# Performance work log

Hardware: AMD Instinct MI355X
Metric: run time of the kernel (lower is better)

Reference implementation:

```python
import jax, jax.numpy as jnp
import numpy as np

B, T, N, C = 1, 2, 10000, 64
H, Co = 4, 64
E = 160000
NEG_SLOPE = 0.2
LN_EPS = 1e-5


def setup_inputs() -> dict:
    key = jax.random.key(0)
    ks = jax.random.split(key, 8)
    s_in = 1.0 / np.sqrt(C)
    s_att = 1.0 / np.sqrt(Co)
    s_proj = 1.0 / np.sqrt(H * Co)
    return {
        "x": jax.random.normal(ks[0], (B, T, N, C), jnp.float32),
        "edge_index": jax.random.randint(ks[1], (2, E), 0, N, dtype=jnp.int32),
        "W_l": jax.random.normal(ks[2], (C, H * Co), jnp.float32) * s_in,
        "b_l": jnp.zeros((H * Co,), jnp.float32),
        "W_r": jax.random.normal(ks[3], (C, H * Co), jnp.float32) * s_in,
        "b_r": jnp.zeros((H * Co,), jnp.float32),
        "att": jax.random.normal(ks[4], (H, Co), jnp.float32) * s_att,
        "bias": jnp.zeros((H * Co,), jnp.float32),
        "W_proj": jax.random.normal(ks[5], (H * Co, Co), jnp.float32) * s_proj,
        "b_proj": jnp.zeros((Co,), jnp.float32),
        "ln_gamma": jnp.ones((Co,), jnp.float32),
        "ln_beta": jnp.zeros((Co,), jnp.float32),
    }


def reference(x, edge_index, W_l, b_l, W_r, b_r, att, bias, W_proj, b_proj, ln_gamma, ln_beta):
    src, dst = edge_index[0], edge_index[1]
    # node transforms: [B,T,N,H,Co]
    x_l = (x @ W_l + b_l).reshape(B, T, N, H, Co)
    x_r = (x @ W_r + b_r).reshape(B, T, N, H, Co)
    # per-edge gathers: [B,T,E,H,Co]
    x_j = x_l[:, :, src]  # source-side features (messages)
    x_i = x_r[:, :, dst]  # target-side features
    m = jax.nn.leaky_relu(x_i + x_j, NEG_SLOPE)
    alpha = jnp.einsum('bteho,ho->bteh', m, att)  # [B,T,E,H]
    # segment softmax over edges grouped by target node (edge axis leading)
    a = jnp.moveaxis(alpha, 2, 0)  # [E,B,T,H]
    amax = jax.lax.stop_gradient(jax.ops.segment_max(a, dst, num_segments=N))
    a = jnp.exp(a - amax[dst])
    denom = jax.ops.segment_sum(a, dst, num_segments=N)
    attn = a / denom[dst]  # [E,B,T,H]
    # weighted messages scattered to target nodes
    msg = jnp.moveaxis(x_j, 2, 0) * attn[..., None]  # [E,B,T,H,Co]
    agg = jax.ops.segment_sum(msg, dst, num_segments=N)  # [N,B,T,H,Co]
    out = jnp.moveaxis(agg, 0, 2).reshape(B, T, N, H * Co) + bias
    x_mha = jax.nn.relu(out)
    # projection + identity residual (in_channels == out_channels)
    x_sam = x_mha @ W_proj + b_proj + x
    mu = jnp.mean(x_sam, axis=-1, keepdims=True)
    var = jnp.var(x_sam, axis=-1, keepdims=True)
    y = (x_sam - mu) * jax.lax.rsqrt(var + LN_EPS) * ln_gamma + ln_beta
    return jax.nn.relu(y)
```

## Files before the change

kernel.cpp:

```cpp
#include <hip/hip_runtime.h>

#define T_  2
#define N_  10000
#define C_  64
#define H_  4
#define Co_ 64
#define E_  160000
#define HC_ 256
#define PAD_ 48
#define NEG_SLOPE 0.2f
#define LN_EPS 1e-5f
#define SCAT_BLOCKS (E_ / 256)
#define GEMM_BLOCKS (T_ * N_ / 32)

typedef float v2f __attribute__((ext_vector_type(2)));
typedef unsigned short bfx8 __attribute__((ext_vector_type(8)));

#if __has_builtin(__builtin_elementwise_fma)
#define PKFMA(a, b, c) __builtin_elementwise_fma((a), (b), (c))
#else
#define PKFMA(a, b, c) ((a) * (b) + (c))
#endif

__device__ __forceinline__ v2f v2(float x, float y) { v2f r; r.x = x; r.y = y; return r; }
__device__ __forceinline__ v2f sp(float x) { v2f r; r.x = x; r.y = x; return r; }

__device__ __forceinline__ float bf2f(unsigned short u) {
    return __uint_as_float((unsigned)u << 16);
}
__device__ __forceinline__ unsigned short f2bf(float f) {
    const unsigned u = __float_as_uint(f);
    return (unsigned short)((u + 0x7FFFu + ((u >> 16) & 1u)) >> 16);
}

__device__ __forceinline__ void red8x2(float& p0, float& p1) {
    asm("s_nop 1\n\t"
        "v_add_f32_dpp %0, %0, %0 quad_perm:[1,0,3,2] row_mask:0xf bank_mask:0xf\n\t"
        "v_add_f32_dpp %1, %1, %1 quad_perm:[1,0,3,2] row_mask:0xf bank_mask:0xf\n\t"
        "s_nop 0\n\t"
        "v_add_f32_dpp %0, %0, %0 quad_perm:[2,3,0,1] row_mask:0xf bank_mask:0xf\n\t"
        "v_add_f32_dpp %1, %1, %1 quad_perm:[2,3,0,1] row_mask:0xf bank_mask:0xf\n\t"
        "s_nop 0\n\t"
        "v_add_f32_dpp %0, %0, %0 row_half_mirror row_mask:0xf bank_mask:0xf\n\t"
        "v_add_f32_dpp %1, %1, %1 row_half_mirror row_mask:0xf bank_mask:0xf"
        : "+v"(p0), "+v"(p1));
}

__global__ __launch_bounds__(256) void scat_gemm(
        const int* __restrict__ src, const int* __restrict__ dst,
        int* __restrict__ cursor, unsigned short* __restrict__ perm,
        const float* __restrict__ x, const float* __restrict__ Wl,
        const float* __restrict__ bl, const float* __restrict__ Wr,
        const float* __restrict__ br, unsigned short* __restrict__ xlb,
        float* __restrict__ xr) {
    __shared__ float4 xs[32 * 16];
    const int tid = threadIdx.x;
    if (blockIdx.x < SCAT_BLOCKS) {
        const int e = blockIdx.x * 256 + tid;
        const int d = dst[e];
        const int pos = atomicAdd(&cursor[d], 1);
        if (pos < PAD_) perm[d * PAD_ + pos] = (unsigned short)src[e];
        return;
    }
    const int r0 = (blockIdx.x - SCAT_BLOCKS) * 32;
    xs[tid]       = ((const float4*)(x + (size_t)r0 * C_))[tid];
    xs[256 + tid] = ((const float4*)(x + (size_t)r0 * C_))[256 + tid];
    __syncthreads();

    const int wv    = tid >> 6;
    const int mat   = wv >> 1;
    const int rbase = (wv & 1) << 4;
    const int col4  = tid & 63;
    const float* W  = mat ? Wr : Wl;
    const float4 b4 = ((const float4*)(mat ? br : bl))[col4];

    v2f accA[16], accB[16];
    #pragma unroll
    for (int r = 0; r < 16; ++r) { accA[r] = v2(b4.x, b4.y); accB[r] = v2(b4.z, b4.w); }

    #pragma unroll 2
    for (int c4 = 0; c4 < 16; ++c4) {
        const float4 w0 = ((const float4*)(W + (size_t)(c4 * 4 + 0) * HC_))[col4];
        const float4 w1 = ((const float4*)(W + (size_t)(c4 * 4 + 1) * HC_))[col4];
        const float4 w2 = ((const float4*)(W + (size_t)(c4 * 4 + 2) * HC_))[col4];
        const float4 w3 = ((const float4*)(W + (size_t)(c4 * 4 + 3) * HC_))[col4];
        const v2f w0A = v2(w0.x, w0.y), w0B = v2(w0.z, w0.w);
        const v2f w1A = v2(w1.x, w1.y), w1B = v2(w1.z, w1.w);
        const v2f w2A = v2(w2.x, w2.y), w2B = v2(w2.z, w2.w);
        const v2f w3A = v2(w3.x, w3.y), w3B = v2(w3.z, w3.w);
        #pragma unroll
        for (int r = 0; r < 16; ++r) {
            const float4 xv = xs[(rbase + r) * 16 + c4];
            accA[r] = PKFMA(sp(xv.x), w0A, accA[r]);
            accB[r] = PKFMA(sp(xv.x), w0B, accB[r]);
            accA[r] = PKFMA(sp(xv.y), w1A, accA[r]);
            accB[r] = PKFMA(sp(xv.y), w1B, accB[r]);
            accA[r] = PKFMA(sp(xv.z), w2A, accA[r]);
            accB[r] = PKFMA(sp(xv.z), w2B, accB[r]);
            accA[r] = PKFMA(sp(xv.w), w3A, accA[r]);
            accB[r] = PKFMA(sp(xv.w), w3B, accB[r]);
        }
    }
    if (mat) {
        #pragma unroll
        for (int r = 0; r < 16; ++r) {
            float4 o4;
            o4.x = accA[r].x; o4.y = accA[r].y; o4.z = accB[r].x; o4.w = accB[r].y;
            ((float4*)(xr + (size_t)(r0 + rbase + r) * HC_))[col4] = o4;
        }
    } else {
        #pragma unroll
        for (int r = 0; r < 16; ++r) {
            ushort4 u;
            u.x = f2bf(accA[r].x); u.y = f2bf(accA[r].y);
            u.z = f2bf(accB[r].x); u.w = f2bf(accB[r].y);
            ((ushort4*)(xlb + (size_t)(r0 + rbase + r) * HC_))[col4] = u;
        }
    }
}

__global__ __launch_bounds__(128, 6) void node_proj(
        const unsigned short* __restrict__ xlb, const float* __restrict__ xr,
        const float* __restrict__ att, const unsigned short* __restrict__ perm,
        const int* __restrict__ cursor, const float* __restrict__ bias,
        const float* __restrict__ Wp, const float* __restrict__ bp,
        const float* __restrict__ x, const float* __restrict__ gamma,
        const float* __restrict__ beta, float* __restrict__ out) {
    __shared__ float sh_act[T_][HC_];
    __shared__ float sh_part[T_][T_][Co_];
    const int t    = threadIdx.x >> 6;
    const int lane = threadIdx.x & 63;
    const int q    = lane & 31;
    const int half = lane >> 5;
    const int n    = blockIdx.x;
    const int deg  = min(cursor[n], PAD_);
    const int lim  = deg - half;
    const size_t row = (size_t)t * N_ + n;

    const float4 xiA = ((const float4*)&xr[row * HC_])[2 * q];
    const float4 xiB = ((const float4*)&xr[row * HC_])[2 * q + 1];
    const float4 avA = ((const float4*)att)[2 * q];
    const float4 avB = ((const float4*)att)[2 * q + 1];
    const v2f X0 = v2(xiA.x, xiA.y), X1 = v2(xiA.z, xiA.w);
    const v2f X2 = v2(xiB.x, xiB.y), X3 = v2(xiB.z, xiB.w);
    const float L2E = 1.44269504f;
    const v2f A0v = v2(avA.x * L2E, avA.y * L2E), A1v = v2(avA.z * L2E, avA.w * L2E);
    const v2f A2v = v2(avB.x * L2E, avB.y * L2E), A3v = v2(avB.z * L2E, avB.w * L2E);

    const int myidx = (lane < deg) ? (int)perm[n * PAD_ + lane] : 0;
    const unsigned short* xlt = xlb + (size_t)t * N_ * HC_;

    float s = 0.f;
    v2f ac0 = v2(0.f, 0.f), ac1 = ac0, ac2 = ac0, ac3 = ac0;

    bfx8 Au, Bu, Cu, Du;
    auto fetchA = [&](int kk) {
        const int i0 = __builtin_amdgcn_readlane(myidx, kk + 0);
        const int i1 = __builtin_amdgcn_readlane(myidx, kk + 1);
        const int i2 = __builtin_amdgcn_readlane(myidx, kk + 2);
        const int i3 = __builtin_amdgcn_readlane(myidx, kk + 3);
        const int ia = half ? i1 : i0;
        const int ib = half ? i3 : i2;
        Au = *(const bfx8*)&xlt[(size_t)ia * HC_ + 8 * q];
        Bu = *(const bfx8*)&xlt[(size_t)ib * HC_ + 8 * q];
    };
    auto fetchB = [&](int kk) {
        const int i0 = __builtin_amdgcn_readlane(myidx, kk + 0);
        const int i1 = __builtin_amdgcn_readlane(myidx, kk + 1);
        const int i2 = __builtin_amdgcn_readlane(myidx, kk + 2);
        const int i3 = __builtin_amdgcn_readlane(myidx, kk + 3);
        const int ia = half ? i1 : i0;
        const int ib = half ? i3 : i2;
        Cu = *(const bfx8*)&xlt[(size_t)ia * HC_ + 8 * q];
        Du = *(const bfx8*)&xlt[(size_t)ib * HC_ + 8 * q];
    };
    auto pair_update = [&](const bfx8 u0, const bfx8 u1, int kbase) {
        const v2f c00 = v2(bf2f(u0[0]), bf2f(u0[1]));
        const v2f c01 = v2(bf2f(u0[2]), bf2f(u0[3]));
        const v2f c02 = v2(bf2f(u0[4]), bf2f(u0[5]));
        const v2f c03 = v2(bf2f(u0[6]), bf2f(u0[7]));
        const v2f c10 = v2(bf2f(u1[0]), bf2f(u1[1]));
        const v2f c11 = v2(bf2f(u1[2]), bf2f(u1[3]));
        const v2f c12 = v2(bf2f(u1[4]), bf2f(u1[5]));
        const v2f c13 = v2(bf2f(u1[6]), bf2f(u1[7]));
        v2f u, l, P;
        u = c00 + X0; l = __builtin_elementwise_max(u, u * NEG_SLOPE); P = l * A0v;
        u = c01 + X1; l = __builtin_elementwise_max(u, u * NEG_SLOPE); P = PKFMA(l, A1v, P);
        u = c02 + X2; l = __builtin_elementwise_max(u, u * NEG_SLOPE); P = PKFMA(l, A2v, P);
        u = c03 + X3; l = __builtin_elementwise_max(u, u * NEG_SLOPE); P = PKFMA(l, A3v, P);
        float p0 = P.x + P.y;
        u = c10 + X0; l = __builtin_elementwise_max(u, u * NEG_SLOPE); P = l * A0v;
        u = c11 + X1; l = __builtin_elementwise_max(u, u * NEG_SLOPE); P = PKFMA(l, A1v, P);
        u = c12 + X2; l = __builtin_elementwise_max(u, u * NEG_SLOPE); P = PKFMA(l, A2v, P);
        u = c13 + X3; l = __builtin_elementwise_max(u, u * NEG_SLOPE); P = PKFMA(l, A3v, P);
        float p1 = P.x + P.y;
        p0 = (kbase < lim)     ? p0 : -INFINITY;
        p1 = (kbase + 2 < lim) ? p1 : -INFINITY;
        red8x2(p0, p1);
        const float w0 = exp2f(p0);
        const float w1 = exp2f(p1);
        s += w0 + w1;
        ac0 = PKFMA(c00, sp(w0), ac0); ac0 = PKFMA(c10, sp(w1), ac0);
        ac1 = PKFMA(c01, sp(w0), ac1); ac1 = PKFMA(c11, sp(w1), ac1);
        ac2 = PKFMA(c02, sp(w0), ac2); ac2 = PKFMA(c12, sp(w1), ac2);
        ac3 = PKFMA(c03, sp(w0), ac3); ac3 = PKFMA(c13, sp(w1), ac3);
    };
    if (deg > 0) fetchA(0);
    if (deg > 4) fetchB(4);
    for (int k = 0; k < deg; k += 8) {
        {
            const bfx8 u0 = Au, u1 = Bu;
            if (k + 8 < deg) fetchA(k + 8);
            pair_update(u0, u1, k);
        }
        if (k + 4 < deg) {
            const bfx8 u0 = Cu, u1 = Du;
            if (k + 12 < deg) fetchB(k + 12);
            pair_update(u0, u1, k + 4);
        }
    }

    s += __shfl_xor(s, 32, 64);
    ac0.x += __shfl_xor(ac0.x, 32, 64); ac0.y += __shfl_xor(ac0.y, 32, 64);
    ac1.x += __shfl_xor(ac1.x, 32, 64); ac1.y += __shfl_xor(ac1.y, 32, 64);
    ac2.x += __shfl_xor(ac2.x, 32, 64); ac2.y += __shfl_xor(ac2.y, 32, 64);
    ac3.x += __shfl_xor(ac3.x, 32, 64); ac3.y += __shfl_xor(ac3.y, 32, 64);

    if (lane < 32) {
        const float inv = (deg > 0) ? 1.f / s : 0.f;
        const float4 bA = ((const float4*)bias)[2 * q];
        const float4 bB = ((const float4*)bias)[2 * q + 1];
        float4 vA, vB;
        vA.x = fmaxf(fmaf(ac0.x, inv, bA.x), 0.f);
        vA.y = fmaxf(fmaf(ac0.y, inv, bA.y), 0.f);
        vA.z = fmaxf(fmaf(ac1.x, inv, bA.z), 0.f);
        vA.w = fmaxf(fmaf(ac1.y, inv, bA.w), 0.f);
        vB.x = fmaxf(fmaf(ac2.x, inv, bB.x), 0.f);
        vB.y = fmaxf(fmaf(ac2.y, inv, bB.y), 0.f);
        vB.z = fmaxf(fmaf(ac3.x, inv, bB.z), 0.f);
        vB.w = fmaxf(fmaf(ac3.y, inv, bB.w), 0.f);
        ((float4*)&sh_act[t][0])[2 * q]     = vA;
        ((float4*)&sh_act[t][0])[2 * q + 1] = vB;
    }
    __syncthreads();

    v2f P0 = v2(0.f, 0.f), P1 = v2(0.f, 0.f);
    {
        const int kq = t * 32;
        #pragma unroll 4
        for (int k4 = 0; k4 < 32; ++k4) {
            const int k = (kq + k4) * 4;
            const float w0 = Wp[(size_t)(k + 0) * Co_ + lane];
            const float w1 = Wp[(size_t)(k + 1) * Co_ + lane];
            const float w2 = Wp[(size_t)(k + 2) * Co_ + lane];
            const float w3 = Wp[(size_t)(k + 3) * Co_ + lane];
            const v2f w01 = v2(w0, w1), w23 = v2(w2, w3);
            const float4 a0 = ((const float4*)&sh_act[0][0])[kq + k4];
            const float4 a1 = ((const float4*)&sh_act[1][0])[kq + k4];
            P0 = PKFMA(v2(a0.x, a0.y), w01, P0);
            P0 = PKFMA(v2(a0.z, a0.w), w23, P0);
            P1 = PKFMA(v2(a1.x, a1.y), w01, P1);
            P1 = PKFMA(v2(a1.z, a1.w), w23, P1);
        }
    }
    sh_part[t][0][lane] = P0.x + P0.y;
    sh_part[t][1][lane] = P1.x + P1.y;
    __syncthreads();

    const int o = lane;
    float p = sh_part[0][t][o] + sh_part[1][t][o]
            + bp[o] + x[((size_t)t * N_ + n) * C_ + o];
    const float go = gamma[o], bo = beta[o];
    float s1r = p;
    #pragma unroll
    for (int off = 1; off < 64; off <<= 1) s1r += __shfl_xor(s1r, off, 64);
    const float mu = s1r * (1.f / 64.f);
    const float dv = p - mu;
    float s2r = dv * dv;
    #pragma unroll
    for (int off = 1; off < 64; off <<= 1) s2r += __shfl_xor(s2r, off, 64);
    out[((size_t)t * N_ + n) * C_ + o] =
        fmaxf(dv * rsqrtf(s2r * (1.f / 64.f) + LN_EPS) * go + bo, 0.f);
}

extern "C" void kernel_launch(void* const* d_in, const int* in_sizes, int n_in,
                              void* d_out, int out_size, void* d_ws, size_t ws_size,
                              hipStream_t stream) {
    const float* x    = (const float*)d_in[0];
    const int*   ei   = (const int*)  d_in[1];
    const float* Wl   = (const float*)d_in[2];
    const float* bl   = (const float*)d_in[3];
    const float* Wr   = (const float*)d_in[4];
    const float* br   = (const float*)d_in[5];
    const float* att  = (const float*)d_in[6];
    const float* bias = (const float*)d_in[7];
    const float* Wp   = (const float*)d_in[8];
    const float* bp   = (const float*)d_in[9];
    const float* gam  = (const float*)d_in[10];
    const float* bet  = (const float*)d_in[11];
    const int* src = ei;
    const int* dst = ei + E_;

    char* ws = (char*)d_ws;
    unsigned short* xlb  = (unsigned short*)ws;
    float*          xr   = (float*)(xlb + (size_t)T_ * N_ * HC_);
    int*            cursor = (int*)(xr + (size_t)T_ * N_ * HC_);
    unsigned short* perm   = (unsigned short*)(cursor + N_);

    hipMemsetAsync(cursor, 0, N_ * sizeof(int), stream);
    scat_gemm<<<SCAT_BLOCKS + GEMM_BLOCKS, 256, 0, stream>>>(
        src, dst, cursor, perm, x, Wl, bl, Wr, br, xlb, xr);
    node_proj<<<N_, 128, 0, stream>>>(xlb, xr, att, perm, cursor, bias,
                                      Wp, bp, x, gam, bet, (float*)d_out);
}
```

Before: 158.9 us.

## Deepen gather prefetch to three stages and pre-transpose projection weights

```diff
diff --git a/kernel.cpp b/kernel.cpp
--- a/kernel.cpp
+++ b/kernel.cpp
@@ -52,7 +52,8 @@
         const float* __restrict__ x, const float* __restrict__ Wl,
         const float* __restrict__ bl, const float* __restrict__ Wr,
         const float* __restrict__ br, unsigned short* __restrict__ xlb,
-        float* __restrict__ xr) {
+        float* __restrict__ xr, const float* __restrict__ Wp,
+        float* __restrict__ WpT) {
     __shared__ float4 xs[32 * 16];
     const int tid = threadIdx.x;
     if (blockIdx.x < SCAT_BLOCKS) {
@@ -60,6 +61,12 @@
         const int d = dst[e];
         const int pos = atomicAdd(&cursor[d], 1);
         if (pos < PAD_) perm[d * PAD_ + pos] = (unsigned short)src[e];
+        return;
+    }
+    if (blockIdx.x >= SCAT_BLOCKS + GEMM_BLOCKS) {
+        const int o = tid & 63, kb = (tid >> 6) * 64;
+        for (int k = kb; k < kb + 64; ++k)
+            WpT[(size_t)o * HC_ + k] = Wp[(size_t)k * Co_ + o];
         return;
     }
     const int r0 = (blockIdx.x - SCAT_BLOCKS) * 32;
@@ -119,11 +126,11 @@
     }
 }
 
-__global__ __launch_bounds__(128, 6) void node_proj(
+__global__ __launch_bounds__(128, 8) void node_proj(
         const unsigned short* __restrict__ xlb, const float* __restrict__ xr,
         const float* __restrict__ att, const unsigned short* __restrict__ perm,
         const int* __restrict__ cursor, const float* __restrict__ bias,
-        const float* __restrict__ Wp, const float* __restrict__ bp,
+        const float* __restrict__ WpT, const float* __restrict__ bp,
         const float* __restrict__ x, const float* __restrict__ gamma,
         const float* __restrict__ beta, float* __restrict__ out) {
     __shared__ float sh_act[T_][HC_];
@@ -153,7 +160,7 @@
     float s = 0.f;
     v2f ac0 = v2(0.f, 0.f), ac1 = ac0, ac2 = ac0, ac3 = ac0;
 
-    bfx8 Au, Bu, Cu, Du;
+    bfx8 Au, Bu, Cu, Du, Eu, Fu;
     auto fetchA = [&](int kk) {
         const int i0 = __builtin_amdgcn_readlane(myidx, kk + 0);
         const int i1 = __builtin_amdgcn_readlane(myidx, kk + 1);
@@ -173,6 +180,16 @@
         const int ib = half ? i3 : i2;
         Cu = *(const bfx8*)&xlt[(size_t)ia * HC_ + 8 * q];
         Du = *(const bfx8*)&xlt[(size_t)ib * HC_ + 8 * q];
+    };
+    auto fetchC = [&](int kk) {
+        const int i0 = __builtin_amdgcn_readlane(myidx, kk + 0);
+        const int i1 = __builtin_amdgcn_readlane(myidx, kk + 1);
+        const int i2 = __builtin_amdgcn_readlane(myidx, kk + 2);
+        const int i3 = __builtin_amdgcn_readlane(myidx, kk + 3);
+        const int ia = half ? i1 : i0;
+        const int ib = half ? i3 : i2;
+        Eu = *(const bfx8*)&xlt[(size_t)ia * HC_ + 8 * q];
+        Fu = *(const bfx8*)&xlt[(size_t)ib * HC_ + 8 * q];
     };
     auto pair_update = [&](const bfx8 u0, const bfx8 u1, int kbase) {
         const v2f c00 = v2(bf2f(u0[0]), bf2f(u0[1]));
@@ -207,16 +224,22 @@
     };
     if (deg > 0) fetchA(0);
     if (deg > 4) fetchB(4);
-    for (int k = 0; k < deg; k += 8) {
+    if (deg > 8) fetchC(8);
+    for (int k = 0; k < deg; k += 12) {
         {
             const bfx8 u0 = Au, u1 = Bu;
-            if (k + 8 < deg) fetchA(k + 8);
+            if (k + 12 < deg) fetchA(k + 12);
             pair_update(u0, u1, k);
         }
         if (k + 4 < deg) {
             const bfx8 u0 = Cu, u1 = Du;
-            if (k + 12 < deg) fetchB(k + 12);
+            if (k + 16 < deg) fetchB(k + 16);
             pair_update(u0, u1, k + 4);
+        }
+        if (k + 8 < deg) {
+            const bfx8 u0 = Eu, u1 = Fu;
+            if (k + 20 < deg) fetchC(k + 20);
+            pair_update(u0, u1, k + 8);
         }
     }
 
@@ -246,21 +269,17 @@
 
     v2f P0 = v2(0.f, 0.f), P1 = v2(0.f, 0.f);
     {
+        const float* wrow = WpT + (size_t)lane * HC_ + t * 128;
         const int kq = t * 32;
         #pragma unroll 4
         for (int k4 = 0; k4 < 32; ++k4) {
-            const int k = (kq + k4) * 4;
-            const float w0 = Wp[(size_t)(k + 0) * Co_ + lane];
-            const float w1 = Wp[(size_t)(k + 1) * Co_ + lane];
-            const float w2 = Wp[(size_t)(k + 2) * Co_ + lane];
-            const float w3 = Wp[(size_t)(k + 3) * Co_ + lane];
-            const v2f w01 = v2(w0, w1), w23 = v2(w2, w3);
+            const float4 w  = ((const float4*)wrow)[k4];
             const float4 a0 = ((const float4*)&sh_act[0][0])[kq + k4];
             const float4 a1 = ((const float4*)&sh_act[1][0])[kq + k4];
-            P0 = PKFMA(v2(a0.x, a0.y), w01, P0);
-            P0 = PKFMA(v2(a0.z, a0.w), w23, P0);
-            P1 = PKFMA(v2(a1.x, a1.y), w01, P1);
-            P1 = PKFMA(v2(a1.z, a1.w), w23, P1);
+            P0 = PKFMA(v2(a0.x, a0.y), v2(w.x, w.y), P0);
+            P0 = PKFMA(v2(a0.z, a0.w), v2(w.z, w.w), P0);
+            P1 = PKFMA(v2(a1.x, a1.y), v2(w.x, w.y), P1);
+            P1 = PKFMA(v2(a1.z, a1.w), v2(w.z, w.w), P1);
         }
     }
     sh_part[t][0][lane] = P0.x + P0.y;
@@ -306,10 +325,11 @@
     float*          xr   = (float*)(xlb + (size_t)T_ * N_ * HC_);
     int*            cursor = (int*)(xr + (size_t)T_ * N_ * HC_);
     unsigned short* perm   = (unsigned short*)(cursor + N_);
+    float*          WpT    = (float*)(perm + (size_t)N_ * PAD_);
 
     hipMemsetAsync(cursor, 0, N_ * sizeof(int), stream);
-    scat_gemm<<<SCAT_BLOCKS + GEMM_BLOCKS, 256, 0, stream>>>(
-        src, dst, cursor, perm, x, Wl, bl, Wr, br, xlb, xr);
+    scat_gemm<<<SCAT_BLOCKS + GEMM_BLOCKS + 1, 256, 0, stream>>>(
+        src, dst, cursor, perm, x, Wl, bl, Wr, br, xlb, xr, Wp, WpT);
     node_proj<<<N_, 128, 0, stream>>>(xlb, xr, att, perm, cursor, bias,
-                                      Wp, bp, x, gam, bet, (float*)d_out);
-}
+                                      WpT, bp, x, gam, bet, (float*)d_out);
+}
```

Result: slower. 274.6 us (+72.8%).
